# Performance work log

Hardware: AMD Instinct MI355X
Metric: run time of the kernel (lower is better)

Reference implementation:

```python
import jax, jax.numpy as jnp
import numpy as np

B, D, H, E, TOP_K = 4096, 1024, 4096, 8, 2
EPS = 2.220446049250313e-16  # float64 machine eps, as in the torch source


def setup_inputs() -> dict:
    key = jax.random.key(0)
    k0, k1, k2, k3 = jax.random.split(key, 4)
    x = jax.random.normal(k0, (B, 1, D), dtype=jnp.float32)
    # torch inits w_gate to zeros (degenerate ties in topk); use small random for a meaningful test
    w_gate = jax.random.normal(k1, (D, E), dtype=jnp.float32) * 0.02
    W1 = jax.random.normal(k2, (E, D, H), dtype=jnp.float32) * (1.0 / np.sqrt(D))
    b1 = jnp.zeros((E, H), dtype=jnp.float32)
    W2 = jax.random.normal(k3, (E, H, D), dtype=jnp.float32) * (1.0 / np.sqrt(H))
    b2 = jnp.zeros((E, D), dtype=jnp.float32)
    loss_coef = jnp.float32(0.01)
    return {"x": x, "w_gate": w_gate, "W1": W1, "b1": b1, "W2": W2, "b2": b2,
            "loss_coef": loss_coef}


def _cv_squared(v, eps=1e-10):
    # torch .var() is unbiased (ddof=1)
    return jnp.var(v, ddof=1) / (jnp.mean(v) ** 2 + eps)


def reference(x, w_gate, W1, b1, W2, b2, loss_coef):
    n_tok = x.shape[0]
    flat = x.reshape(n_tok, -1)                      # [B, D]

    # --- top-k gating ---
    logits = flat @ w_gate                           # [B, E]
    top_logits, top_idx = jax.lax.top_k(logits, TOP_K)
    top_gates = jax.nn.softmax(top_logits, axis=1)   # softmax over the top-k logits only
    gates = jnp.zeros_like(logits).at[jnp.arange(n_tok)[:, None], top_idx].set(top_gates)

    # --- load-balancing loss ---
    importance = gates.sum(axis=0)                               # [E]
    load = (gates > 0).sum(axis=0).astype(jnp.float32)           # [E]
    balancing_loss = (_cv_squared(importance) + _cv_squared(load)) * loss_coef

    # --- per-expert FFN (dense equivalent of sort/dispatch: zero gates kill non-routed terms) ---
    h = jax.nn.relu(jnp.einsum('bd,edh->beh', flat, W1) + b1)    # [B, E, H]
    o = jnp.einsum('beh,ehd->bed', h, W2) + b2                   # [B, E, D]

    # --- combine: sum_e gate * exp(expert_out), then log (exp/log trick) ---
    combined = jnp.einsum('bed,be->bd', jnp.exp(o), gates)       # [B, D]
    combined = jnp.where(combined == 0, EPS, combined)
    y = jnp.log(combined)
    return y, balancing_loss
```

## Files before the change

kernel.cpp:

```cpp
#include <hip/hip_runtime.h>


typedef __attribute__((ext_vector_type(8))) short short8;
typedef __attribute__((ext_vector_type(4))) float f32x4;

#define B_TOK 4096
#define D_DIM 1024
#define H_DIM 4096
#define N_EXP 8
#define H_HALF 2048

__device__ __forceinline__ unsigned short f2bf(float f) {
  unsigned int u = __float_as_uint(f);
  u += 0x7fffu + ((u >> 16) & 1u);
  return (unsigned short)(u >> 16);
}
__device__ __forceinline__ float bf2f(unsigned short s) {
  return __uint_as_float(((unsigned int)s) << 16);
}

__device__ __forceinline__ void async_ld16(const void* g, void* l) {
  __builtin_amdgcn_global_load_lds(
      (const __attribute__((address_space(1))) void*)g,
      (__attribute__((address_space(3))) void*)l, 16, 0, 0);
}

__global__ __launch_bounds__(256) void convert_x_kernel(const float* __restrict__ x,
                                                        unsigned short* __restrict__ xb) {
  const size_t i = ((size_t)blockIdx.x * 256 + threadIdx.x) * 4;
  float4 v = *(const float4*)(x + i);
  ushort4 r;
  r.x = f2bf(v.x); r.y = f2bf(v.y); r.z = f2bf(v.z); r.w = f2bf(v.w);
  *(ushort4*)(xb + i) = r;
}

__global__ __launch_bounds__(256) void gating_kernel(
    const float* __restrict__ x, const float* __restrict__ wg,
    int* __restrict__ tok_e, float* __restrict__ tok_g) {
  const int lane = threadIdx.x & 63;
  const int t = blockIdx.x * 4 + (threadIdx.x >> 6);
  const float* xr = x + (size_t)t * D_DIM;
  double acc[8] = {0, 0, 0, 0, 0, 0, 0, 0};
  for (int d = lane; d < D_DIM; d += 64) {
    double xv = (double)xr[d];
    const float4 w0 = *(const float4*)(wg + d * 8);
    const float4 w1 = *(const float4*)(wg + d * 8 + 4);
    acc[0] += xv * (double)w0.x; acc[1] += xv * (double)w0.y;
    acc[2] += xv * (double)w0.z; acc[3] += xv * (double)w0.w;
    acc[4] += xv * (double)w1.x; acc[5] += xv * (double)w1.y;
    acc[6] += xv * (double)w1.z; acc[7] += xv * (double)w1.w;
  }
#pragma unroll
  for (int e = 0; e < 8; ++e) {
    double v = acc[e];
#pragma unroll
    for (int m = 32; m > 0; m >>= 1) v += __shfl_xor(v, m, 64);
    acc[e] = v;
  }
  if (lane == 0) {
    double b1v = -1e300, b2v = -1e300;
    int i1 = 0, i2 = 0;
#pragma unroll
    for (int e = 0; e < 8; ++e) {
      double v = acc[e];
      if (v > b1v) { b2v = b1v; i2 = i1; b1v = v; i1 = e; }
      else if (v > b2v) { b2v = v; i2 = e; }
    }
    float ex = expf((float)b2v - (float)b1v);
    float den = 1.f + ex;
    tok_e[2 * t] = i1; tok_e[2 * t + 1] = i2;
    tok_g[2 * t] = 1.f / den; tok_g[2 * t + 1] = ex / den;
  }
}

__global__ __launch_bounds__(1024) void route_kernel(
    const int* __restrict__ tok_e, const float* __restrict__ tok_g,
    int* __restrict__ tok_p, int* __restrict__ bucket,
    int* __restrict__ counts, int* __restrict__ offs,
    const float* __restrict__ coef, float* __restrict__ loss_out) {
  __shared__ int wavecnt[16][8];
  __shared__ int wavebase[16][8];
  __shared__ int run[8];
  __shared__ float impl[8];
  const int tid = threadIdx.x, lane = tid & 63, wv = tid >> 6;
  if (tid < 8) { run[tid] = 0; impl[tid] = 0.f; }
  __syncthreads();
  for (int c = 0; c < 8; ++c) {
    const int i = c * 1024 + tid;
    const int e = tok_e[i];
    const float g = tok_g[i];
    int rank = 0;
#pragma unroll
    for (int ee = 0; ee < 8; ++ee) {
      unsigned long long m = __ballot(e == ee);
      if (e == ee) rank = __popcll(m & ((1ull << lane) - 1ull));
      float s = (e == ee) ? g : 0.f;
#pragma unroll
      for (int o = 32; o > 0; o >>= 1) s += __shfl_xor(s, o, 64);
      if (lane == 0) {
        wavecnt[wv][ee] = __popcll(m);
        impl[ee] += 0.f;
        atomicAdd(&impl[ee], s);
      }
    }
    __syncthreads();
    if (tid < 8) {
      int base = run[tid];
      for (int w = 0; w < 16; ++w) { wavebase[w][tid] = base; base += wavecnt[w][tid]; }
      run[tid] = base;
    }
    __syncthreads();
    const int pos = wavebase[wv][e] + rank;
    tok_p[i] = pos;
    bucket[e * B_TOK + pos] = i >> 1;
  }
  __syncthreads();
  if (tid == 0) {
    int o = 0;
    double mi = 0, ml = 0;
    for (int e = 0; e < 8; ++e) {
      counts[e] = run[e]; offs[e] = o; o += run[e];
      mi += (double)impl[e]; ml += (double)run[e];
    }
    offs[8] = o;
    mi *= 0.125; ml *= 0.125;
    double vi = 0, vl = 0;
    for (int e = 0; e < 8; ++e) {
      double di = (double)impl[e] - mi; vi += di * di;
      double dl = (double)run[e]  - ml; vl += dl * dl;
    }
    vi /= 7.0; vl /= 7.0;
    *loss_out = (float)((vi / (mi * mi + 1e-10) + vl / (ml * ml + 1e-10)) * (double)coef[0]);
  }
}

__global__ __launch_bounds__(256) void transpose_w_kernel(
    const float* __restrict__ W, unsigned short* __restrict__ Wt,
    int ND_src, int k_base, int n_base, int KD_out,
    size_t w_stride_e, size_t wt_stride_e) {
  const int e = blockIdx.z;
  const int kt = blockIdx.x * 64;
  const int nt = blockIdx.y * 64;
  const float* We = W + (size_t)e * w_stride_e + (size_t)(k_base + kt) * ND_src + n_base + nt;
  unsigned short* Wte = Wt + (size_t)e * wt_stride_e + (size_t)nt * KD_out + kt;
  __shared__ unsigned int Ul[64][36];
  const int t = threadIdx.x;
  const int cb = (t & 15) * 4;
#pragma unroll
  for (int j = 0; j < 2; ++j) {
    const int p = (t >> 4) + j * 16;
    float4 f0 = *(const float4*)(We + (size_t)(2 * p) * ND_src + cb);
    float4 f1 = *(const float4*)(We + (size_t)(2 * p + 1) * ND_src + cb);
#pragma unroll
    for (int i2 = 0; i2 < 4; ++i2) {
      unsigned int u = (unsigned int)f2bf(((const float*)&f0)[i2]) |
                       ((unsigned int)f2bf(((const float*)&f1)[i2]) << 16);
      Ul[cb + i2][p] = u;
    }
  }
  __syncthreads();
  const int on = t >> 2;
  const int om = (t & 3) * 8;
  uint4 a = *(const uint4*)&Ul[on][om];
  uint4 b = *(const uint4*)&Ul[on][om + 4];
  uint4* dst = (uint4*)(Wte + (size_t)on * KD_out + om * 2);
  dst[0] = a; dst[1] = b;
}

template <int KDIM, int NDIM, bool GATHER, bool RELU, bool ACCUM>
__global__ __launch_bounds__(256) void grouped_gemm(
    const unsigned short* __restrict__ A, const unsigned short* __restrict__ Bt,
    const float* __restrict__ bias, int biasN,
    const int* __restrict__ counts, const int* __restrict__ offs,
    const int* __restrict__ bucket, unsigned short* __restrict__ Out, int outN) {
  const int e = blockIdx.z;
  const int n_e = counts[e];
  const int row0 = blockIdx.y * 128;
  if (row0 >= n_e) return;
  const int m_cnt = min(128, n_e - row0);
  const int n0 = blockIdx.x * 128;
  const int slot0 = offs[e] + row0;

  __shared__ unsigned short Alds[128][32];
  __shared__ unsigned short Blds[128][32];
  __shared__ int toklds[128];

  const int tid = threadIdx.x;
  const int lane = tid & 63;
  const int wid = tid >> 6;
  const int q = lane >> 4, l15 = lane & 15;
  const int wm = (wid >> 1) * 64, wn = (wid & 1) * 64;

  if (GATHER) {
    if (tid < 128) toklds[tid] = bucket[e * B_TOK + row0 + min(tid, m_cnt - 1)];
    __syncthreads();
  }
  const int r0 = tid >> 2;
  const int kc = (tid & 3) * 8;
  size_t ga0, ga1;
  if (GATHER) {
    ga0 = (size_t)toklds[r0] * KDIM + kc;
    ga1 = (size_t)toklds[r0 + 64] * KDIM + kc;
  } else {
    ga0 = (size_t)(slot0 + min(r0, m_cnt - 1)) * KDIM + kc;
    ga1 = (size_t)(slot0 + min(r0 + 64, m_cnt - 1)) * KDIM + kc;
  }
  const unsigned short* bbase =
      Bt + (size_t)e * NDIM * KDIM + (size_t)(n0 + r0) * KDIM + kc;
  char* aldsw = (char*)Alds + wid * 1024;
  char* bldsw = (char*)Blds + wid * 1024;

  f32x4 acc[4][4] = {};
  for (int k0 = 0; k0 < KDIM; k0 += 32) {
    async_ld16(A + ga0 + k0, aldsw);
    async_ld16(A + ga1 + k0, aldsw + 4096);
    async_ld16(bbase + k0, bldsw);
    async_ld16(bbase + (size_t)64 * KDIM + k0, bldsw + 4096);
    __syncthreads();
    short8 af[4], bfr[4];
#pragma unroll
    for (int mi = 0; mi < 4; ++mi) af[mi] = *(const short8*)&Alds[wm + mi * 16 + l15][q * 8];
#pragma unroll
    for (int ni = 0; ni < 4; ++ni) bfr[ni] = *(const short8*)&Blds[wn + ni * 16 + l15][q * 8];
#pragma unroll
    for (int mi = 0; mi < 4; ++mi)
#pragma unroll
      for (int ni = 0; ni < 4; ++ni)
        acc[mi][ni] = __builtin_amdgcn_mfma_f32_16x16x32_bf16(af[mi], bfr[ni], acc[mi][ni], 0, 0, 0);
    __syncthreads();
  }

  const float* be = bias + (size_t)e * biasN + n0;
#pragma unroll
  for (int ni = 0; ni < 4; ++ni) {
    const int c = wn + ni * 16 + l15;
    const float bv = ACCUM ? 0.f : be[c];
#pragma unroll
    for (int mi = 0; mi < 4; ++mi) {
      const int rb = wm + mi * 16 + q * 4;
#pragma unroll
      for (int rg = 0; rg < 4; ++rg) {
        const int r = rb + rg;
        if (r < m_cnt) {
          float v = acc[mi][ni][rg] + bv;
          if (RELU) v = fmaxf(v, 0.f);
          unsigned short* op = Out + (size_t)(slot0 + r) * outN + n0 + c;
          if (ACCUM) v += bf2f(*op);
          *op = f2bf(v);
        }
      }
    }
  }
}

__device__ __forceinline__ float comb1(float a, float b, float g1, float g2) {
  float c = g1 * expf(a) + g2 * expf(b);
  if (c == 0.f) c = 2.220446049250313e-16f;
  return logf(c);
}

__global__ __launch_bounds__(256) void combine_kernel(
    const unsigned short* __restrict__ o_buf, const int* __restrict__ offs,
    const int* __restrict__ tok_e, const int* __restrict__ tok_p,
    const float* __restrict__ tok_g, float* __restrict__ y) {
  const int t = blockIdx.x;
  const int e1 = tok_e[2 * t], e2 = tok_e[2 * t + 1];
  const int s1 = offs[e1] + tok_p[2 * t];
  const int s2 = offs[e2] + tok_p[2 * t + 1];
  const float g1 = tok_g[2 * t], g2 = tok_g[2 * t + 1];
  const int i = threadIdx.x * 4;
  ushort4 a4 = *(const ushort4*)(o_buf + (size_t)s1 * D_DIM + i);
  ushort4 b4 = *(const ushort4*)(o_buf + (size_t)s2 * D_DIM + i);
  float4 r;
  r.x = comb1(bf2f(a4.x), bf2f(b4.x), g1, g2);
  r.y = comb1(bf2f(a4.y), bf2f(b4.y), g1, g2);
  r.z = comb1(bf2f(a4.z), bf2f(b4.z), g1, g2);
  r.w = comb1(bf2f(a4.w), bf2f(b4.w), g1, g2);
  *(float4*)(y + (size_t)t * D_DIM + i) = r;
}

extern "C" void kernel_launch(void* const* d_in, const int* in_sizes, int n_in,
                              void* d_out, int out_size, void* d_ws, size_t ws_size,
                              hipStream_t stream) {
  const float* x  = (const float*)d_in[0];
  const float* wg = (const float*)d_in[1];
  const float* W1 = (const float*)d_in[2];
  const float* b1 = (const float*)d_in[3];
  const float* W2 = (const float*)d_in[4];
  const float* b2 = (const float*)d_in[5];
  const float* cf = (const float*)d_in[6];
  float* y = (float*)d_out;

  char* w = (char*)d_ws;
  unsigned short* x_bf = (unsigned short*)(w);
  int*   counts = (int*)(w + 8388608);
  int*   offs   = (int*)(w + 8388672);
  int*   tok_e  = (int*)(w + 8388736);
  int*   tok_p  = (int*)(w + 8421504);
  float* tok_g  = (float*)(w + 8454272);
  int*   bucket = (int*)(w + 8487040);
  unsigned short* wt     = (unsigned short*)(w + 8618112);
  unsigned short* h_half = (unsigned short*)(w + 42172544);
  unsigned short* o_buf  = (unsigned short*)(w + 75726976);
  if (ws_size < 92504192) return;

  convert_x_kernel<<<4096, 256, 0, stream>>>(x, x_bf);
  gating_kernel<<<1024, 256, 0, stream>>>(x, wg, tok_e, tok_g);
  route_kernel<<<1, 1024, 0, stream>>>(tok_e, tok_g, tok_p, bucket, counts, offs,
                                       cf, y + (size_t)B_TOK * D_DIM);

  for (int p = 0; p < 2; ++p) {
    transpose_w_kernel<<<dim3(16, 32, 8), 256, 0, stream>>>(
        W1, wt, H_DIM, 0, p * H_HALF, D_DIM,
        (size_t)D_DIM * H_DIM, (size_t)H_HALF * D_DIM);
    grouped_gemm<D_DIM, H_HALF, true, true, false>
        <<<dim3(H_HALF / 128, 32, N_EXP), 256, 0, stream>>>(
            x_bf, wt, b1 + p * H_HALF, H_DIM, counts, offs, bucket, h_half, H_HALF);
    transpose_w_kernel<<<dim3(32, 16, 8), 256, 0, stream>>>(
        W2, wt, D_DIM, p * H_HALF, 0, H_HALF,
        (size_t)H_DIM * D_DIM, (size_t)D_DIM * H_HALF);
    if (p == 0)
      grouped_gemm<H_HALF, D_DIM, false, false, false>
          <<<dim3(D_DIM / 128, 32, N_EXP), 256, 0, stream>>>(
              h_half, wt, b2, D_DIM, counts, offs, bucket, o_buf, D_DIM);
    else
      grouped_gemm<H_HALF, D_DIM, false, false, true>
          <<<dim3(D_DIM / 128, 32, N_EXP), 256, 0, stream>>>(
              h_half, wt, b2, D_DIM, counts, offs, bucket, o_buf, D_DIM);
  }

  combine_kernel<<<4096, 256, 0, stream>>>(o_buf, offs, tok_e, tok_p, tok_g, y);
}
```

Baseline: 663.0 us.

## Fuse x conversion into gating, compact tile table, deepen K tile with swizzled LDS

Folds the bf16 conversion of x into the gating kernel, so one launch and one read of x go away. The route kernel now builds a compact table of (expert, row-tile) pairs, and the grouped GEMMs launch over 72 tiles instead of 32x8 mostly-empty blocks. The GEMM K step grows from 32 to 64 with an XOR-swizzled LDS layout to cut bank conflicts and halve the number of barriers. The transpose kernel's LDS padding changes to 33 and its reads become scalar. This doubles LDS per block and relies on 72 tiles being enough for any routing (sum of ceil(count/128) is at most 64+8).

```diff
diff --git a/kernel.cpp b/kernel.cpp
--- a/kernel.cpp
+++ b/kernel.cpp
@@ -25,30 +25,31 @@
       (__attribute__((address_space(3))) void*)l, 16, 0, 0);
 }
 
-__global__ __launch_bounds__(256) void convert_x_kernel(const float* __restrict__ x,
-                                                        unsigned short* __restrict__ xb) {
-  const size_t i = ((size_t)blockIdx.x * 256 + threadIdx.x) * 4;
-  float4 v = *(const float4*)(x + i);
-  ushort4 r;
-  r.x = f2bf(v.x); r.y = f2bf(v.y); r.z = f2bf(v.z); r.w = f2bf(v.w);
-  *(ushort4*)(xb + i) = r;
-}
-
 __global__ __launch_bounds__(256) void gating_kernel(
     const float* __restrict__ x, const float* __restrict__ wg,
-    int* __restrict__ tok_e, float* __restrict__ tok_g) {
+    unsigned short* __restrict__ xb, int* __restrict__ tok_e,
+    float* __restrict__ tok_g) {
   const int lane = threadIdx.x & 63;
   const int t = blockIdx.x * 4 + (threadIdx.x >> 6);
   const float* xr = x + (size_t)t * D_DIM;
   double acc[8] = {0, 0, 0, 0, 0, 0, 0, 0};
-  for (int d = lane; d < D_DIM; d += 64) {
-    double xv = (double)xr[d];
-    const float4 w0 = *(const float4*)(wg + d * 8);
-    const float4 w1 = *(const float4*)(wg + d * 8 + 4);
-    acc[0] += xv * (double)w0.x; acc[1] += xv * (double)w0.y;
-    acc[2] += xv * (double)w0.z; acc[3] += xv * (double)w0.w;
-    acc[4] += xv * (double)w1.x; acc[5] += xv * (double)w1.y;
-    acc[6] += xv * (double)w1.z; acc[7] += xv * (double)w1.w;
+#pragma unroll
+  for (int i = 0; i < 4; ++i) {
+    const int d = i * 256 + lane * 4;
+    float4 xv = *(const float4*)(xr + d);
+    ushort4 xo;
+    xo.x = f2bf(xv.x); xo.y = f2bf(xv.y); xo.z = f2bf(xv.z); xo.w = f2bf(xv.w);
+    *(ushort4*)(xb + (size_t)t * D_DIM + d) = xo;
+#pragma unroll
+    for (int c = 0; c < 4; ++c) {
+      double xd = (double)((const float*)&xv)[c];
+      const float4 w0 = *(const float4*)(wg + (size_t)(d + c) * 8);
+      const float4 w1 = *(const float4*)(wg + (size_t)(d + c) * 8 + 4);
+      acc[0] += xd * (double)w0.x; acc[1] += xd * (double)w0.y;
+      acc[2] += xd * (double)w0.z; acc[3] += xd * (double)w0.w;
+      acc[4] += xd * (double)w1.x; acc[5] += xd * (double)w1.y;
+      acc[6] += xd * (double)w1.z; acc[7] += xd * (double)w1.w;
+    }
   }
 #pragma unroll
   for (int e = 0; e < 8; ++e) {
@@ -77,6 +78,7 @@
     const int* __restrict__ tok_e, const float* __restrict__ tok_g,
     int* __restrict__ tok_p, int* __restrict__ bucket,
     int* __restrict__ counts, int* __restrict__ offs,
+    int* __restrict__ tile_tab, int* __restrict__ ntiles,
     const float* __restrict__ coef, float* __restrict__ loss_out) {
   __shared__ int wavecnt[16][8];
   __shared__ int wavebase[16][8];
@@ -99,7 +101,6 @@
       for (int o = 32; o > 0; o >>= 1) s += __shfl_xor(s, o, 64);
       if (lane == 0) {
         wavecnt[wv][ee] = __popcll(m);
-        impl[ee] += 0.f;
         atomicAdd(&impl[ee], s);
       }
     }
@@ -116,13 +117,16 @@
   }
   __syncthreads();
   if (tid == 0) {
-    int o = 0;
+    int o = 0, T = 0;
     double mi = 0, ml = 0;
     for (int e = 0; e < 8; ++e) {
       counts[e] = run[e]; offs[e] = o; o += run[e];
       mi += (double)impl[e]; ml += (double)run[e];
+      const int nt = (run[e] + 127) >> 7;
+      for (int yt = 0; yt < nt; ++yt) tile_tab[T++] = (e << 16) | yt;
     }
     offs[8] = o;
+    ntiles[0] = T;
     mi *= 0.125; ml *= 0.125;
     double vi = 0, vl = 0;
     for (int e = 0; e < 8; ++e) {
@@ -143,7 +147,7 @@
   const int nt = blockIdx.y * 64;
   const float* We = W + (size_t)e * w_stride_e + (size_t)(k_base + kt) * ND_src + n_base + nt;
   unsigned short* Wte = Wt + (size_t)e * wt_stride_e + (size_t)nt * KD_out + kt;
-  __shared__ unsigned int Ul[64][36];
+  __shared__ unsigned int Ul[64][33];
   const int t = threadIdx.x;
   const int cb = (t & 15) * 4;
 #pragma unroll
@@ -153,18 +157,17 @@
     float4 f1 = *(const float4*)(We + (size_t)(2 * p + 1) * ND_src + cb);
 #pragma unroll
     for (int i2 = 0; i2 < 4; ++i2) {
-      unsigned int u = (unsigned int)f2bf(((const float*)&f0)[i2]) |
+      Ul[cb + i2][p] = (unsigned int)f2bf(((const float*)&f0)[i2]) |
                        ((unsigned int)f2bf(((const float*)&f1)[i2]) << 16);
-      Ul[cb + i2][p] = u;
     }
   }
   __syncthreads();
-  const int on = t >> 2;
-  const int om = (t & 3) * 8;
-  uint4 a = *(const uint4*)&Ul[on][om];
-  uint4 b = *(const uint4*)&Ul[on][om + 4];
+  const int on = t >> 2, om = (t & 3) * 8;
+  union { unsigned int u[8]; uint4 v[2]; } o;
+#pragma unroll
+  for (int i = 0; i < 8; ++i) o.u[i] = Ul[on][om + i];
   uint4* dst = (uint4*)(Wte + (size_t)on * KD_out + om * 2);
-  dst[0] = a; dst[1] = b;
+  dst[0] = o.v[0]; dst[1] = o.v[1];
 }
 
 template <int KDIM, int NDIM, bool GATHER, bool RELU, bool ACCUM>
@@ -172,17 +175,19 @@
     const unsigned short* __restrict__ A, const unsigned short* __restrict__ Bt,
     const float* __restrict__ bias, int biasN,
     const int* __restrict__ counts, const int* __restrict__ offs,
-    const int* __restrict__ bucket, unsigned short* __restrict__ Out, int outN) {
-  const int e = blockIdx.z;
+    const int* __restrict__ bucket, const int* __restrict__ tile_tab,
+    const int* __restrict__ ntiles, unsigned short* __restrict__ Out, int outN) {
+  if ((int)blockIdx.y >= ntiles[0]) return;
+  const int te = tile_tab[blockIdx.y];
+  const int e = te >> 16;
+  const int row0 = (te & 0xffff) << 7;
   const int n_e = counts[e];
-  const int row0 = blockIdx.y * 128;
-  if (row0 >= n_e) return;
   const int m_cnt = min(128, n_e - row0);
   const int n0 = blockIdx.x * 128;
   const int slot0 = offs[e] + row0;
 
-  __shared__ unsigned short Alds[128][32];
-  __shared__ unsigned short Blds[128][32];
+  __shared__ unsigned short Alds[128][64];
+  __shared__ unsigned short Blds[128][64];
   __shared__ int toklds[128];
 
   const int tid = threadIdx.x;
@@ -195,38 +200,48 @@
     if (tid < 128) toklds[tid] = bucket[e * B_TOK + row0 + min(tid, m_cnt - 1)];
     __syncthreads();
   }
-  const int r0 = tid >> 2;
-  const int kc = (tid & 3) * 8;
-  size_t ga0, ga1;
-  if (GATHER) {
-    ga0 = (size_t)toklds[r0] * KDIM + kc;
-    ga1 = (size_t)toklds[r0 + 64] * KDIM + kc;
-  } else {
-    ga0 = (size_t)(slot0 + min(r0, m_cnt - 1)) * KDIM + kc;
-    ga1 = (size_t)(slot0 + min(r0 + 64, m_cnt - 1)) * KDIM + kc;
-  }
-  const unsigned short* bbase =
-      Bt + (size_t)e * NDIM * KDIM + (size_t)(n0 + r0) * KDIM + kc;
-  char* aldsw = (char*)Alds + wid * 1024;
-  char* bldsw = (char*)Blds + wid * 1024;
+
+  unsigned int ga[4], gb[4];
+#pragma unroll
+  for (int i = 0; i < 4; ++i) {
+    const int c = i * 256 + tid;
+    const int r = c >> 3;
+    const int cl = (c & 7) ^ (r & 7);
+    int arow;
+    if (GATHER) arow = toklds[r];
+    else arow = slot0 + min(r, m_cnt - 1);
+    ga[i] = (unsigned int)arow * KDIM + cl * 8;
+    gb[i] = (unsigned int)(n0 + r) * KDIM + cl * 8;
+  }
+  const unsigned short* Be = Bt + (size_t)e * NDIM * KDIM;
 
   f32x4 acc[4][4] = {};
-  for (int k0 = 0; k0 < KDIM; k0 += 32) {
-    async_ld16(A + ga0 + k0, aldsw);
-    async_ld16(A + ga1 + k0, aldsw + 4096);
-    async_ld16(bbase + k0, bldsw);
-    async_ld16(bbase + (size_t)64 * KDIM + k0, bldsw + 4096);
-    __syncthreads();
-    short8 af[4], bfr[4];
-#pragma unroll
-    for (int mi = 0; mi < 4; ++mi) af[mi] = *(const short8*)&Alds[wm + mi * 16 + l15][q * 8];
-#pragma unroll
-    for (int ni = 0; ni < 4; ++ni) bfr[ni] = *(const short8*)&Blds[wn + ni * 16 + l15][q * 8];
-#pragma unroll
-    for (int mi = 0; mi < 4; ++mi)
-#pragma unroll
-      for (int ni = 0; ni < 4; ++ni)
-        acc[mi][ni] = __builtin_amdgcn_mfma_f32_16x16x32_bf16(af[mi], bfr[ni], acc[mi][ni], 0, 0, 0);
+  for (int k0 = 0; k0 < KDIM; k0 += 64) {
+#pragma unroll
+    for (int i = 0; i < 4; ++i) {
+      async_ld16(A + (size_t)ga[i] + k0, (char*)Alds + i * 4096 + wid * 1024);
+      async_ld16(Be + (size_t)gb[i] + k0, (char*)Blds + i * 4096 + wid * 1024);
+    }
+    __syncthreads();
+#pragma unroll
+    for (int kk = 0; kk < 2; ++kk) {
+      short8 af[4], bfr[4];
+#pragma unroll
+      for (int mi = 0; mi < 4; ++mi) {
+        const int R = wm + mi * 16 + l15;
+        af[mi] = *(const short8*)&Alds[R][((4 * kk + q) ^ (R & 7)) * 8];
+      }
+#pragma unroll
+      for (int ni = 0; ni < 4; ++ni) {
+        const int R = wn + ni * 16 + l15;
+        bfr[ni] = *(const short8*)&Blds[R][((4 * kk + q) ^ (R & 7)) * 8];
+      }
+#pragma unroll
+      for (int mi = 0; mi < 4; ++mi)
+#pragma unroll
+        for (int ni = 0; ni < 4; ++ni)
+          acc[mi][ni] = __builtin_amdgcn_mfma_f32_16x16x32_bf16(af[mi], bfr[ni], acc[mi][ni], 0, 0, 0);
+    }
     __syncthreads();
   }
 
@@ -293,40 +308,45 @@
 
   char* w = (char*)d_ws;
   unsigned short* x_bf = (unsigned short*)(w);
-  int*   counts = (int*)(w + 8388608);
-  int*   offs   = (int*)(w + 8388672);
-  int*   tok_e  = (int*)(w + 8388736);
-  int*   tok_p  = (int*)(w + 8421504);
-  float* tok_g  = (float*)(w + 8454272);
-  int*   bucket = (int*)(w + 8487040);
-  unsigned short* wt     = (unsigned short*)(w + 8618112);
-  unsigned short* h_half = (unsigned short*)(w + 42172544);
-  unsigned short* o_buf  = (unsigned short*)(w + 75726976);
-  if (ws_size < 92504192) return;
-
-  convert_x_kernel<<<4096, 256, 0, stream>>>(x, x_bf);
-  gating_kernel<<<1024, 256, 0, stream>>>(x, wg, tok_e, tok_g);
+  int*   counts   = (int*)(w + 8388608);
+  int*   offs     = (int*)(w + 8388672);
+  int*   ntiles   = (int*)(w + 8388736);
+  int*   tile_tab = (int*)(w + 8388800);
+  int*   tok_e    = (int*)(w + 8389632);
+  int*   tok_p    = (int*)(w + 8422400);
+  float* tok_g    = (float*)(w + 8455168);
+  int*   bucket   = (int*)(w + 8487936);
+  unsigned short* wt     = (unsigned short*)(w + 8619008);
+  unsigned short* h_half = (unsigned short*)(w + 42173440);
+  unsigned short* o_buf  = (unsigned short*)(w + 75727872);
+  if (ws_size < 92505088) return;
+
+  gating_kernel<<<1024, 256, 0, stream>>>(x, wg, x_bf, tok_e, tok_g);
   route_kernel<<<1, 1024, 0, stream>>>(tok_e, tok_g, tok_p, bucket, counts, offs,
-                                       cf, y + (size_t)B_TOK * D_DIM);
+                                       tile_tab, ntiles, cf,
+                                       y + (size_t)B_TOK * D_DIM);
 
   for (int p = 0; p < 2; ++p) {
     transpose_w_kernel<<<dim3(16, 32, 8), 256, 0, stream>>>(
         W1, wt, H_DIM, 0, p * H_HALF, D_DIM,
         (size_t)D_DIM * H_DIM, (size_t)H_HALF * D_DIM);
     grouped_gemm<D_DIM, H_HALF, true, true, false>
-        <<<dim3(H_HALF / 128, 32, N_EXP), 256, 0, stream>>>(
-            x_bf, wt, b1 + p * H_HALF, H_DIM, counts, offs, bucket, h_half, H_HALF);
+        <<<dim3(H_HALF / 128, 72, 1), 256, 0, stream>>>(
+            x_bf, wt, b1 + p * H_HALF, H_DIM, counts, offs, bucket,
+            tile_tab, ntiles, h_half, H_HALF);
     transpose_w_kernel<<<dim3(32, 16, 8), 256, 0, stream>>>(
         W2, wt, D_DIM, p * H_HALF, 0, H_HALF,
         (size_t)H_DIM * D_DIM, (size_t)D_DIM * H_HALF);
     if (p == 0)
       grouped_gemm<H_HALF, D_DIM, false, false, false>
-          <<<dim3(D_DIM / 128, 32, N_EXP), 256, 0, stream>>>(
-              h_half, wt, b2, D_DIM, counts, offs, bucket, o_buf, D_DIM);
+          <<<dim3(D_DIM / 128, 72, 1), 256, 0, stream>>>(
+              h_half, wt, b2, D_DIM, counts, offs, bucket,
+              tile_tab, ntiles, o_buf, D_DIM);
     else
       grouped_gemm<H_HALF, D_DIM, false, false, true>
-          <<<dim3(D_DIM / 128, 32, N_EXP), 256, 0, stream>>>(
-              h_half, wt, b2, D_DIM, counts, offs, bucket, o_buf, D_DIM);
+          <<<dim3(D_DIM / 128, 72, 1), 256, 0, stream>>>(
+              h_half, wt, b2, D_DIM, counts, offs, bucket,
+              tile_tab, ntiles, o_buf, D_DIM);
   }
 
   combine_kernel<<<4096, 256, 0, stream>>>(o_buf, offs, tok_e, tok_p, tok_g, y);
```

Measured after the change: 727.2 us. 1.1x slower.
